# Performance work log

Measured on AMD Instinct MI355X. Metric: run time of the kernel, lower is better.

## Reference

```python
import jax, jax.numpy as jnp
import numpy as np

B, S, D, H = 4, 1024, 1024, 16
HD = D // H


def setup_inputs() -> dict:
    key = jax.random.key(0)
    ks = jax.random.split(key, 8)
    q = jax.random.normal(ks[0], (B, S, D), jnp.float32)
    q_mask = jnp.ones((B, S), dtype=bool)
    kv_mask = jax.random.randint(ks[1], (B, S), 0, 2).astype(bool)
    edge_weights = jax.random.uniform(ks[2], (B, S, S), jnp.float32)
    w_init = 0.02
    wq = jax.random.normal(ks[3], (D, D), jnp.float32) * w_init
    wk = jax.random.normal(ks[4], (D, D), jnp.float32) * w_init
    wv = jax.random.normal(ks[5], (D, D), jnp.float32) * w_init
    wo = jax.random.normal(ks[6], (D, D), jnp.float32) * w_init
    bo = jnp.zeros((D,), jnp.float32)
    return {"q": q, "q_mask": q_mask, "kv_mask": kv_mask,
            "edge_weights": edge_weights, "wq": wq, "wk": wk, "wv": wv,
            "wo": wo, "bo": bo}


def _pass_with_mask(x, w, mask, b=None):
    # Linear applied everywhere, padded rows zeroed (matches pass_with_mask)
    y = x @ w.T
    if b is not None:
        y = y + b
    return jnp.where(mask[..., None], y, 0.0)


def reference(q, q_mask, kv_mask, edge_weights, wq, wk, wv, wo, bo):
    b = q.shape[0]
    # merge_masks: padding mask outer product (recv x send)
    full_mask = (q_mask[:, :, None] & kv_mask[:, None, :])[:, None]  # [b,1,s,s]
    # projections (self attention: k = v = q)
    qh = _pass_with_mask(q, wq, q_mask).reshape(b, S, H, HD).transpose(0, 2, 1, 3)
    kh = _pass_with_mask(q, wk, kv_mask).reshape(b, S, H, HD).transpose(0, 2, 1, 3)
    vh = _pass_with_mask(q, wv, kv_mask).reshape(b, S, H, HD).transpose(0, 2, 1, 3)
    # NOTE: faithful to source, scaled by sqrt(model_dim), not sqrt(head_dim)
    scores = jnp.einsum("bhqd,bhkd->bhqk", qh, kh) / np.sqrt(D).astype(np.float32)
    scores = scores * edge_weights[:, None]          # mul_weights=True
    scores = jnp.where(full_mask, scores, -jnp.inf)
    scores = jax.nn.softmax(scores, axis=-1)
    scores = jnp.where(full_mask, scores, 0.0)       # re-zero masked entries
    out = jnp.einsum("bhqk,bhkd->bhqd", scores, vh)
    out = out.transpose(0, 2, 1, 3).reshape(b, S, D)
    return _pass_with_mask(out, wo, q_mask, bo)
```

## Files before the change

kernel.cpp:

```cpp
#include <hip/hip_runtime.h>

typedef unsigned short u16;
typedef unsigned int u32;
typedef __bf16 b16x8 __attribute__((ext_vector_type(8)));
typedef u16 u16x8 __attribute__((ext_vector_type(8)));
typedef float f32x4 __attribute__((ext_vector_type(4)));
typedef float f32x16 __attribute__((ext_vector_type(16)));
typedef u32 u32x2 __attribute__((ext_vector_type(2)));

#define DEV __device__ __forceinline__
#define INF __builtin_inff()
#define MFMA16(a, b, c) __builtin_amdgcn_mfma_f32_16x16x32_bf16((a), (b), (c), 0, 0, 0)
#define MFMA32(a, b, c) __builtin_amdgcn_mfma_f32_32x32x16_bf16((a), (b), (c), 0, 0, 0)
#define EXP2F(x) __builtin_amdgcn_exp2f(x)

DEV u16 f2b(float f) {
  union { float f; unsigned u; } x; x.f = f;
  unsigned r = x.u + 0x7fffu + ((x.u >> 16) & 1u);
  return (u16)(r >> 16);
}

DEV u32 pk2(float a, float b) {
  __bf16 lo = (__bf16)a, hi = (__bf16)b;
  u16 ul, uh;
  __builtin_memcpy(&ul, &lo, 2);
  __builtin_memcpy(&uh, &hi, 2);
  return (u32)ul | ((u32)uh << 16);
}

DEV float b2f(u16 v) {
  union { u32 u; float f; } x; x.u = (u32)v << 16; return x.f;
}

DEV void gl_lds16(const u16* g, u16* l) {
  __builtin_amdgcn_global_load_lds((const __attribute__((address_space(1))) void*)g,
                                   (__attribute__((address_space(3))) void*)l, 16, 0, 0);
}

__global__ __launch_bounds__(256) void prep_all(const float* __restrict__ q,
                                                const float* __restrict__ wq,
                                                const float* __restrict__ wk,
                                                const float* __restrict__ wv,
                                                const float* __restrict__ wo,
                                                const float* __restrict__ edge,
                                                u16* __restrict__ xb, u16* __restrict__ wqb,
                                                u16* __restrict__ wkb, u16* __restrict__ wvb,
                                                u16* __restrict__ wob, u16* __restrict__ Ef) {
  __shared__ float Ls[32][132];
  const int blk = blockIdx.x;
  const int tid = threadIdx.x;
  if (blk < 8192) {
    const float* src; u16* dst; float scale = 1.f; int base;
    if (blk < 4096)      { src = q;  dst = xb;  base = blk; }
    else if (blk < 5120) { src = wq; dst = wqb; base = blk - 4096; scale = 0.045084441f; }
    else if (blk < 6144) { src = wk; dst = wkb; base = blk - 5120; }
    else if (blk < 7168) { src = wv; dst = wvb; base = blk - 6144; }
    else                 { src = wo; dst = wob; base = blk - 7168; }
    const int i = base * 256 + tid;
    float4 v = reinterpret_cast<const float4*>(src)[i];
    ushort4 o;
    o.x = f2b(v.x * scale);
    o.y = f2b(v.y * scale);
    o.z = f2b(v.z * scale);
    o.w = f2b(v.w * scale);
    reinterpret_cast<ushort4*>(dst)[i] = o;
    return;
  }
  const int rr = blk - 8192;
  const int c = rr & 7, qt = (rr >> 3) & 31, b = rr >> 8;
#pragma unroll
  for (int it = 0; it < 4; ++it) {
    int idx = it * 256 + tid;
    int r = idx >> 5, k4 = idx & 31;
    f32x4 v = *reinterpret_cast<const f32x4*>(
        edge + (size_t)(b * 1024 + qt * 32 + r) * 1024 + c * 128 + k4 * 4);
    *reinterpret_cast<f32x4*>(&Ls[r][k4 * 4]) = v;
  }
  __syncthreads();
#pragma unroll
  for (int it = 0; it < 2; ++it) {
    int slot = it * 256 + tid;
    int kvtl = slot >> 7, i = (slot >> 6) & 1, lane = slot & 63;
    int qv = lane & 31, hi = lane >> 5;
    u16x8 o;
#pragma unroll
    for (int jp = 0; jp < 8; ++jp) {
      int j = i * 8 + jp;
      int kvl = (j & 3) + 8 * (j >> 2) + 4 * hi;
      o[jp] = f2b(Ls[qv][kvtl * 32 + kvl]);
    }
    *reinterpret_cast<u16x8*>(
        Ef + ((size_t)(b * 32 + qt) * 32 + (c * 4 + kvtl)) * 1024 + i * 512 + lane * 8) = o;
  }
}

template <int MODE>
DEV void gemm_body(u16* __restrict__ SA, u16* __restrict__ SB, int m0, int n0,
                   const u16* __restrict__ A, const u16* __restrict__ W,
                   u16* __restrict__ Ybf, float* __restrict__ Yf,
                   const float* __restrict__ bias, const int* __restrict__ qmask) {
  const int t = threadIdx.x;
  const int lane = t & 63, w = t >> 6;
  const int lr = lane & 15, lg = lane >> 4;
  const int wr = w >> 1, wc = w & 1;

  f32x4 acc[4][4] = {};

  const int r0 = t >> 2;
  const int xw = (r0 >> 1) & 3;
  const int c0 = (((t & 3) ^ xw)) * 8;
  const int xa = (lr >> 1) & 3;
  const u16* gA = A + (size_t)(m0 + r0) * 1024 + c0;
  const u16* gB = W + (size_t)(n0 + r0) * 1024 + c0;

  auto stage = [&](int buf, int kt) {
    const int ko = kt * 32;
    u16* lA = SA + buf * 4096 + w * 512;
    u16* lB = SB + buf * 4096 + w * 512;
    gl_lds16(gA + ko, lA);
    gl_lds16(gA + ko + 64 * 1024, lA + 2048);
    gl_lds16(gB + ko, lB);
    gl_lds16(gB + ko + 64 * 1024, lB + 2048);
  };

  stage(0, 0);
  __syncthreads();
  for (int kt = 0; kt < 32; ++kt) {
    const int cur = kt & 1;
    if (kt < 31) stage(cur ^ 1, kt + 1);
    const u16* As = SA + cur * 4096;
    const u16* Bs = SB + cur * 4096;
    b16x8 af[4], bf[4];
#pragma unroll
    for (int m = 0; m < 4; ++m)
      af[m] = *reinterpret_cast<const b16x8*>(As + (wr * 64 + m * 16 + lr) * 32 + ((lg ^ xa) * 8));
#pragma unroll
    for (int n = 0; n < 4; ++n)
      bf[n] = *reinterpret_cast<const b16x8*>(Bs + (wc * 64 + n * 16 + lr) * 32 + ((lg ^ xa) * 8));
#pragma unroll
    for (int m = 0; m < 4; ++m)
#pragma unroll
      for (int n = 0; n < 4; ++n)
        acc[m][n] = MFMA16(af[m], bf[n], acc[m][n]);
    __syncthreads();
  }

#pragma unroll
  for (int m = 0; m < 4; ++m) {
    const int row = m0 + wr * 64 + m * 16 + lg * 4;
#pragma unroll
    for (int n = 0; n < 4; ++n) {
      const int col = n0 + wc * 64 + n * 16 + lr;
#pragma unroll
      for (int r = 0; r < 4; ++r) {
        const int rowg = row + r;
        const float v = acc[m][n][r];
        if (MODE == 3) {
          float y = v + bias[col];
          Yf[(size_t)rowg * 1024 + col] = qmask[rowg] ? y : 0.f;
        } else if (MODE == 1) {
          const int bb = rowg >> 10, rw = rowg & 1023, rt = rw >> 5, rl = rw & 31;
          const int h = col >> 6, dh = col & 63;
          const int s = dh >> 4, hi = (dh >> 3) & 1, j = dh & 7;
          size_t idx = (((size_t)((bb * 16 + h) * 32 + rt) * 4 + s) * 64 + (rl + (hi << 5))) * 8 + j;
          Ybf[idx] = f2b(v);
        } else {
          const int bb = rowg >> 10, kv = rowg & 1023, kvt = kv >> 5, kvl = kv & 31;
          const int s = kvl >> 4, k16 = kvl & 15;
          const int hi = (k16 >> 2) & 1;
          const int j = (k16 & 3) | (((k16 >> 3) & 1) << 2);
          const int h = col >> 6, dh = col & 63, d = dh >> 5;
          size_t idx = ((((size_t)((bb * 16 + h) * 32 + kvt) * 2 + d) * 2 + s) * 64 + ((dh & 31) + (hi << 5))) * 8 + j;
          Ybf[idx] = f2b(v);
        }
      }
    }
  }
}

__global__ __launch_bounds__(256, 4) void gemm_qkv(const u16* __restrict__ X,
                                                   const u16* __restrict__ Wq,
                                                   const u16* __restrict__ Wk,
                                                   const u16* __restrict__ Wv,
                                                   u16* __restrict__ Yq, u16* __restrict__ Yk,
                                                   u16* __restrict__ Yv) {
  __shared__ __attribute__((aligned(16))) u16 SA[2 * 4096];
  __shared__ __attribute__((aligned(16))) u16 SB[2 * 4096];
  const int id = blockIdx.x;
  const int swz = (id & 7) * 96 + (id >> 3);
  const int z = swz >> 8, rem = swz & 255;
  const int by = rem >> 3, bx = rem & 7;
  const int m0 = by * 128, n0 = bx * 128;
  if (z == 0)      gemm_body<1>(SA, SB, m0, n0, X, Wq, Yq, nullptr, nullptr, nullptr);
  else if (z == 1) gemm_body<1>(SA, SB, m0, n0, X, Wk, Yk, nullptr, nullptr, nullptr);
  else             gemm_body<2>(SA, SB, m0, n0, X, Wv, Yv, nullptr, nullptr, nullptr);
}
__global__ __launch_bounds__(256, 4) void gemm_final(const u16* __restrict__ A,
                                                     const u16* __restrict__ Wo,
                                                     float* __restrict__ Out,
                                                     const float* __restrict__ bias,
                                                     const int* __restrict__ qmask) {
  __shared__ __attribute__((aligned(16))) u16 SA[2 * 4096];
  __shared__ __attribute__((aligned(16))) u16 SB[2 * 4096];
  const int id = blockIdx.x;
  const int swz = (id & 7) * 32 + (id >> 3);
  const int by = swz >> 3, bx = swz & 7;
  gemm_body<3>(SA, SB, by * 128, bx * 128, A, Wo, nullptr, Out, bias, qmask);
}

__global__ __launch_bounds__(256, 2) void attn_kernel(
    const u16* __restrict__ Qf, const u16* __restrict__ Kf,
    const u16* __restrict__ Vf, const u16* __restrict__ Ef,
    const int* __restrict__ kvm, u16* __restrict__ out) {
  __shared__ float Osh[3][64][33];
  __shared__ float Lsh[4][32];
  __shared__ __attribute__((aligned(16))) u16 Fsh[1024];

  const int d0 = blockIdx.x;
  const int logical = (d0 & 7) * 256 + (d0 >> 3);
  const int qt = logical & 31, bh = logical >> 5;
  const int b = bh >> 4, h = bh & 15;
  const int tid = threadIdx.x, lane = tid & 63, w = tid >> 6;
  const int ql = lane & 31, hi = lane >> 5;
  const int qrow = qt * 32 + ql;

#pragma unroll
  for (int e = 0; e < 4; ++e) {
    int idx = tid * 4 + e;
    int kt = idx >> 5, h2 = (idx >> 4) & 1, j = idx & 15;
    int kv = kt * 32 + 8 * (j >> 2) + 4 * h2 + (j & 3);
    Fsh[idx] = kvm[b * 1024 + kv] ? (u16)0 : (u16)0xFF80;
  }

  const u16* qp = Qf + (size_t)bh * 65536 + qt * 2048 + lane * 8;
  b16x8 Qr[4];
#pragma unroll
  for (int s = 0; s < 4; ++s) Qr[s] = *reinterpret_cast<const b16x8*>(qp + s * 512);

  const u16* kp = Kf + (size_t)bh * 65536 + lane * 8;
  const u16* vp = Vf + (size_t)bh * 65536 + lane * 8;
  const u16* ep = Ef + (size_t)(b * 32 + qt) * 32768 + lane * 8;

  f32x16 O0 = {}, O1 = {};
  float La[4] = {};

  struct KB { b16x8 K[4]; };
  struct EB { u16x8 E[2]; };
  KB Ka, Kb;
  EB E0, E1, E2, E3;

  auto fK = [&](KB& T, int kvt) {
#pragma unroll
    for (int s = 0; s < 4; ++s)
      T.K[s] = *reinterpret_cast<const b16x8*>(kp + kvt * 2048 + s * 512);
  };
  auto fE = [&](EB& T, int kvt) {
#pragma unroll
    for (int i = 0; i < 2; ++i)
      T.E[i] = *reinterpret_cast<const u16x8*>(ep + kvt * 1024 + i * 512);
  };

  auto compute = [&](const KB& K, const EB& E, int kvt) {
    b16x8 V[4];
#pragma unroll
    for (int ds = 0; ds < 4; ++ds)
      V[ds] = *reinterpret_cast<const b16x8*>(vp + kvt * 2048 + ds * 512);
    u16x8 Fm0 = *reinterpret_cast<const u16x8*>(&Fsh[kvt * 32 + hi * 16]);
    u16x8 Fm1 = *reinterpret_cast<const u16x8*>(&Fsh[kvt * 32 + hi * 16 + 8]);
    f32x16 S = {};
#pragma unroll
    for (int s = 0; s < 4; ++s) S = MFMA32(K.K[s], Qr[s], S);
    float p[16];
#pragma unroll
    for (int j = 0; j < 8; ++j)
      p[j] = EXP2F(fmaf(S[j], b2f(E.E[0][j]), b2f(Fm0[j])));
#pragma unroll
    for (int j = 0; j < 8; ++j)
      p[8 + j] = EXP2F(fmaf(S[8 + j], b2f(E.E[1][j]), b2f(Fm1[j])));
#pragma unroll
    for (int j = 0; j < 16; ++j) La[j & 3] += p[j];
#pragma unroll
    for (int s = 0; s < 2; ++s) {
      union { u32 wd[4]; b16x8 v; } U;
      U.wd[0] = pk2(p[8 * s + 0], p[8 * s + 1]);
      U.wd[1] = pk2(p[8 * s + 2], p[8 * s + 3]);
      U.wd[2] = pk2(p[8 * s + 4], p[8 * s + 5]);
      U.wd[3] = pk2(p[8 * s + 6], p[8 * s + 7]);
      O0 = MFMA32(V[s], U.v, O0);
      O1 = MFMA32(V[2 + s], U.v, O1);
    }
  };

  const int base = w * 8;
  fE(E0, base); fE(E1, base + 1); fE(E2, base + 2);
  fK(Ka, base);
  __syncthreads();

  fE(E3, base + 3); fK(Kb, base + 1); compute(Ka, E0, base + 0);
  fE(E0, base + 4); fK(Ka, base + 2); compute(Kb, E1, base + 1);
  fE(E1, base + 5); fK(Kb, base + 3); compute(Ka, E2, base + 2);
  fE(E2, base + 6); fK(Ka, base + 4); compute(Kb, E3, base + 3);
  fE(E3, base + 7); fK(Kb, base + 5); compute(Ka, E0, base + 4);
                    fK(Ka, base + 6); compute(Kb, E1, base + 5);
                    fK(Kb, base + 7); compute(Ka, E2, base + 6);
                                      compute(Kb, E3, base + 7);

  float Lw = (La[0] + La[1]) + (La[2] + La[3]);
  Lw += __shfl_xor(Lw, 32, 64);

  if (hi == 0) Lsh[w][ql] = Lw;
  if (w > 0) {
#pragma unroll
    for (int r = 0; r < 16; ++r) Osh[w - 1][lane][r] = O0[r];
#pragma unroll
    for (int r = 0; r < 16; ++r) Osh[w - 1][lane][16 + r] = O1[r];
  }
  __syncthreads();
  if (w == 0) {
    float Lg = (Lsh[0][ql] + Lsh[1][ql]) + (Lsh[2][ql] + Lsh[3][ql]);
#pragma unroll
    for (int wv = 0; wv < 3; ++wv) {
#pragma unroll
      for (int r = 0; r < 16; ++r) O0[r] += Osh[wv][lane][r];
#pragma unroll
      for (int r = 0; r < 16; ++r) O1[r] += Osh[wv][lane][16 + r];
    }
    const float inv = (Lg > 0.f) ? 1.f / Lg : 0.f;
    u16* orow = out + (size_t)(b * 1024 + qrow) * 1024 + h * 64 + hi * 4;
#pragma unroll
    for (int H = 0; H < 2; ++H) {
#pragma unroll
      for (int g = 0; g < 4; ++g) {
        float o0 = (H ? O1[4 * g + 0] : O0[4 * g + 0]) * inv;
        float o1 = (H ? O1[4 * g + 1] : O0[4 * g + 1]) * inv;
        float o2 = (H ? O1[4 * g + 2] : O0[4 * g + 2]) * inv;
        float o3 = (H ? O1[4 * g + 3] : O0[4 * g + 3]) * inv;
        u32x2 wv2 = {pk2(o0, o1), pk2(o2, o3)};
        *reinterpret_cast<u32x2*>(orow + H * 32 + g * 8) = wv2;
      }
    }
  }
}

extern "C" void kernel_launch(void* const* d_in, const int* in_sizes, int n_in,
                              void* d_out, int out_size, void* d_ws, size_t ws_size,
                              hipStream_t stream) {
  (void)in_sizes; (void)n_in; (void)out_size; (void)ws_size;
  const float* q    = (const float*)d_in[0];
  const int*   qm   = (const int*)d_in[1];
  const int*   kvm  = (const int*)d_in[2];
  const float* edge = (const float*)d_in[3];
  const float* wq   = (const float*)d_in[4];
  const float* wk   = (const float*)d_in[5];
  const float* wv   = (const float*)d_in[6];
  const float* wo   = (const float*)d_in[7];
  const float* bo   = (const float*)d_in[8];
  float* out = (float*)d_out;

  char* ws = (char*)d_ws;
  u16* xb  = (u16*)(ws);
  u16* wqb = (u16*)(ws + (8ull  << 20));
  u16* wkb = (u16*)(ws + (10ull << 20));
  u16* wvb = (u16*)(ws + (12ull << 20));
  u16* wob = (u16*)(ws + (14ull << 20));
  u16* Qfb = (u16*)(ws + (16ull << 20));
  u16* Kf  = (u16*)(ws + (24ull << 20));
  u16* Vf  = (u16*)(ws + (32ull << 20));
  u16* Ef  = (u16*)(ws + (40ull << 20));
  u16* ab  = xb;

  prep_all<<<9216, 256, 0, stream>>>(q, wq, wk, wv, wo, edge,
                                     xb, wqb, wkb, wvb, wob, Ef);
  gemm_qkv<<<768, 256, 0, stream>>>(xb, wqb, wkb, wvb, Qfb, Kf, Vf);
  attn_kernel<<<2048, 256, 0, stream>>>(Qfb, Kf, Vf, Ef, kvm, ab);
  gemm_final<<<256, 256, 0, stream>>>(ab, wob, out, bo, qm);
}
```

Measured before the change: 112.0 us.

## Move edge-weight repacking into QKV GEMM launch and use 64-row tiles for output GEMM

The edge-weight bf16 repack blocks move out of the conversion kernel and are appended as extra blocks to the QKV GEMM launch, so they run alongside the GEMM tiles instead of serially before them. Shared memory is unified into one buffer so both roles fit. The final output projection becomes a dedicated kernel with 64x128 tiles and 512 blocks instead of 256 blocks of 128x128, giving better CU coverage on a 256-CU part at the cost of reloading each B tile twice as often.

```diff
diff --git a/kernel.cpp b/kernel.cpp
--- a/kernel.cpp
+++ b/kernel.cpp
@@ -37,68 +37,35 @@
                                    (__attribute__((address_space(3))) void*)l, 16, 0, 0);
 }
 
-__global__ __launch_bounds__(256) void prep_all(const float* __restrict__ q,
-                                                const float* __restrict__ wq,
-                                                const float* __restrict__ wk,
-                                                const float* __restrict__ wv,
-                                                const float* __restrict__ wo,
-                                                const float* __restrict__ edge,
-                                                u16* __restrict__ xb, u16* __restrict__ wqb,
-                                                u16* __restrict__ wkb, u16* __restrict__ wvb,
-                                                u16* __restrict__ wob, u16* __restrict__ Ef) {
-  __shared__ float Ls[32][132];
+__global__ __launch_bounds__(256) void cvt_all(const float* __restrict__ q,
+                                               const float* __restrict__ wq,
+                                               const float* __restrict__ wk,
+                                               const float* __restrict__ wv,
+                                               const float* __restrict__ wo,
+                                               u16* __restrict__ xb, u16* __restrict__ wqb,
+                                               u16* __restrict__ wkb, u16* __restrict__ wvb,
+                                               u16* __restrict__ wob) {
   const int blk = blockIdx.x;
-  const int tid = threadIdx.x;
-  if (blk < 8192) {
-    const float* src; u16* dst; float scale = 1.f; int base;
-    if (blk < 4096)      { src = q;  dst = xb;  base = blk; }
-    else if (blk < 5120) { src = wq; dst = wqb; base = blk - 4096; scale = 0.045084441f; }
-    else if (blk < 6144) { src = wk; dst = wkb; base = blk - 5120; }
-    else if (blk < 7168) { src = wv; dst = wvb; base = blk - 6144; }
-    else                 { src = wo; dst = wob; base = blk - 7168; }
-    const int i = base * 256 + tid;
-    float4 v = reinterpret_cast<const float4*>(src)[i];
-    ushort4 o;
-    o.x = f2b(v.x * scale);
-    o.y = f2b(v.y * scale);
-    o.z = f2b(v.z * scale);
-    o.w = f2b(v.w * scale);
-    reinterpret_cast<ushort4*>(dst)[i] = o;
-    return;
-  }
-  const int rr = blk - 8192;
-  const int c = rr & 7, qt = (rr >> 3) & 31, b = rr >> 8;
-#pragma unroll
-  for (int it = 0; it < 4; ++it) {
-    int idx = it * 256 + tid;
-    int r = idx >> 5, k4 = idx & 31;
-    f32x4 v = *reinterpret_cast<const f32x4*>(
-        edge + (size_t)(b * 1024 + qt * 32 + r) * 1024 + c * 128 + k4 * 4);
-    *reinterpret_cast<f32x4*>(&Ls[r][k4 * 4]) = v;
-  }
-  __syncthreads();
-#pragma unroll
-  for (int it = 0; it < 2; ++it) {
-    int slot = it * 256 + tid;
-    int kvtl = slot >> 7, i = (slot >> 6) & 1, lane = slot & 63;
-    int qv = lane & 31, hi = lane >> 5;
-    u16x8 o;
-#pragma unroll
-    for (int jp = 0; jp < 8; ++jp) {
-      int j = i * 8 + jp;
-      int kvl = (j & 3) + 8 * (j >> 2) + 4 * hi;
-      o[jp] = f2b(Ls[qv][kvtl * 32 + kvl]);
-    }
-    *reinterpret_cast<u16x8*>(
-        Ef + ((size_t)(b * 32 + qt) * 32 + (c * 4 + kvtl)) * 1024 + i * 512 + lane * 8) = o;
-  }
+  const float* src; u16* dst; float scale = 1.f; int base;
+  if (blk < 4096)      { src = q;  dst = xb;  base = blk; }
+  else if (blk < 5120) { src = wq; dst = wqb; base = blk - 4096; scale = 0.045084441f; }
+  else if (blk < 6144) { src = wk; dst = wkb; base = blk - 5120; }
+  else if (blk < 7168) { src = wv; dst = wvb; base = blk - 6144; }
+  else                 { src = wo; dst = wob; base = blk - 7168; }
+  const int i = base * 256 + threadIdx.x;
+  float4 v = reinterpret_cast<const float4*>(src)[i];
+  ushort4 o;
+  o.x = f2b(v.x * scale);
+  o.y = f2b(v.y * scale);
+  o.z = f2b(v.z * scale);
+  o.w = f2b(v.w * scale);
+  reinterpret_cast<ushort4*>(dst)[i] = o;
 }
 
 template <int MODE>
 DEV void gemm_body(u16* __restrict__ SA, u16* __restrict__ SB, int m0, int n0,
                    const u16* __restrict__ A, const u16* __restrict__ W,
-                   u16* __restrict__ Ybf, float* __restrict__ Yf,
-                   const float* __restrict__ bias, const int* __restrict__ qmask) {
+                   u16* __restrict__ Ybf) {
   const int t = threadIdx.x;
   const int lane = t & 63, w = t >> 6;
   const int lr = lane & 15, lg = lane >> 4;
@@ -155,10 +122,7 @@
       for (int r = 0; r < 4; ++r) {
         const int rowg = row + r;
         const float v = acc[m][n][r];
-        if (MODE == 3) {
-          float y = v + bias[col];
-          Yf[(size_t)rowg * 1024 + col] = qmask[rowg] ? y : 0.f;
-        } else if (MODE == 1) {
+        if (MODE == 1) {
           const int bb = rowg >> 10, rw = rowg & 1023, rt = rw >> 5, rl = rw & 31;
           const int h = col >> 6, dh = col & 63;
           const int s = dh >> 4, hi = (dh >> 3) & 1, j = dh & 7;
@@ -183,29 +147,122 @@
                                                    const u16* __restrict__ Wk,
                                                    const u16* __restrict__ Wv,
                                                    u16* __restrict__ Yq, u16* __restrict__ Yk,
-                                                   u16* __restrict__ Yv) {
-  __shared__ __attribute__((aligned(16))) u16 SA[2 * 4096];
-  __shared__ __attribute__((aligned(16))) u16 SB[2 * 4096];
+                                                   u16* __restrict__ Yv,
+                                                   const float* __restrict__ edge,
+                                                   u16* __restrict__ Ef) {
+  __shared__ __attribute__((aligned(16))) u16 SU[4 * 4096];
   const int id = blockIdx.x;
+  const int tid = threadIdx.x;
+  if (id >= 768) {
+    float (*Ls)[132] = reinterpret_cast<float(*)[132]>(SU);
+    const int rr = id - 768;
+    const int c = rr & 7, qt = (rr >> 3) & 31, b = rr >> 8;
+#pragma unroll
+    for (int it = 0; it < 4; ++it) {
+      int idx = it * 256 + tid;
+      int r = idx >> 5, k4 = idx & 31;
+      f32x4 v = *reinterpret_cast<const f32x4*>(
+          edge + (size_t)(b * 1024 + qt * 32 + r) * 1024 + c * 128 + k4 * 4);
+      *reinterpret_cast<f32x4*>(&Ls[r][k4 * 4]) = v;
+    }
+    __syncthreads();
+#pragma unroll
+    for (int it = 0; it < 2; ++it) {
+      int slot = it * 256 + tid;
+      int kvtl = slot >> 7, i = (slot >> 6) & 1, lane = slot & 63;
+      int qv = lane & 31, hi = lane >> 5;
+      u16x8 o;
+#pragma unroll
+      for (int jp = 0; jp < 8; ++jp) {
+        int j = i * 8 + jp;
+        int kvl = (j & 3) + 8 * (j >> 2) + 4 * hi;
+        o[jp] = f2b(Ls[qv][kvtl * 32 + kvl]);
+      }
+      *reinterpret_cast<u16x8*>(
+          Ef + ((size_t)(b * 32 + qt) * 32 + (c * 4 + kvtl)) * 1024 + i * 512 + lane * 8) = o;
+    }
+    return;
+  }
+  u16* SA = SU;
+  u16* SB = SU + 2 * 4096;
   const int swz = (id & 7) * 96 + (id >> 3);
   const int z = swz >> 8, rem = swz & 255;
   const int by = rem >> 3, bx = rem & 7;
   const int m0 = by * 128, n0 = bx * 128;
-  if (z == 0)      gemm_body<1>(SA, SB, m0, n0, X, Wq, Yq, nullptr, nullptr, nullptr);
-  else if (z == 1) gemm_body<1>(SA, SB, m0, n0, X, Wk, Yk, nullptr, nullptr, nullptr);
-  else             gemm_body<2>(SA, SB, m0, n0, X, Wv, Yv, nullptr, nullptr, nullptr);
-}
-__global__ __launch_bounds__(256, 4) void gemm_final(const u16* __restrict__ A,
-                                                     const u16* __restrict__ Wo,
-                                                     float* __restrict__ Out,
-                                                     const float* __restrict__ bias,
-                                                     const int* __restrict__ qmask) {
-  __shared__ __attribute__((aligned(16))) u16 SA[2 * 4096];
+  if (z == 0)      gemm_body<1>(SA, SB, m0, n0, X, Wq, Yq);
+  else if (z == 1) gemm_body<1>(SA, SB, m0, n0, X, Wk, Yk);
+  else             gemm_body<2>(SA, SB, m0, n0, X, Wv, Yv);
+}
+
+__global__ __launch_bounds__(256, 4) void gemm_final64(const u16* __restrict__ A,
+                                                       const u16* __restrict__ Wo,
+                                                       float* __restrict__ Out,
+                                                       const float* __restrict__ bias,
+                                                       const int* __restrict__ qmask) {
+  __shared__ __attribute__((aligned(16))) u16 SA[2 * 2048];
   __shared__ __attribute__((aligned(16))) u16 SB[2 * 4096];
   const int id = blockIdx.x;
-  const int swz = (id & 7) * 32 + (id >> 3);
+  const int swz = (id & 7) * 64 + (id >> 3);
   const int by = swz >> 3, bx = swz & 7;
-  gemm_body<3>(SA, SB, by * 128, bx * 128, A, Wo, nullptr, Out, bias, qmask);
+  const int m0 = by * 64, n0 = bx * 128;
+  const int t = threadIdx.x;
+  const int lane = t & 63, w = t >> 6;
+  const int lr = lane & 15, lg = lane >> 4;
+  const int wr = w >> 1, wc = w & 1;
+
+  f32x4 acc[2][4] = {};
+
+  const int r0 = t >> 2;
+  const int xw = (r0 >> 1) & 3;
+  const int c0 = (((t & 3) ^ xw)) * 8;
+  const int xa = (lr >> 1) & 3;
+  const u16* gA = A + (size_t)(m0 + r0) * 1024 + c0;
+  const u16* gB = Wo + (size_t)(n0 + r0) * 1024 + c0;
+
+  auto stage = [&](int buf, int kt) {
+    const int ko = kt * 32;
+    u16* lA = SA + buf * 2048 + w * 512;
+    u16* lB = SB + buf * 4096 + w * 512;
+    gl_lds16(gA + ko, lA);
+    gl_lds16(gB + ko, lB);
+    gl_lds16(gB + ko + 64 * 1024, lB + 2048);
+  };
+
+  stage(0, 0);
+  __syncthreads();
+  for (int kt = 0; kt < 32; ++kt) {
+    const int cur = kt & 1;
+    if (kt < 31) stage(cur ^ 1, kt + 1);
+    const u16* As = SA + cur * 2048;
+    const u16* Bs = SB + cur * 4096;
+    b16x8 af[2], bf[4];
+#pragma unroll
+    for (int m = 0; m < 2; ++m)
+      af[m] = *reinterpret_cast<const b16x8*>(As + (wr * 32 + m * 16 + lr) * 32 + ((lg ^ xa) * 8));
+#pragma unroll
+    for (int n = 0; n < 4; ++n)
+      bf[n] = *reinterpret_cast<const b16x8*>(Bs + (wc * 64 + n * 16 + lr) * 32 + ((lg ^ xa) * 8));
+#pragma unroll
+    for (int m = 0; m < 2; ++m)
+#pragma unroll
+      for (int n = 0; n < 4; ++n)
+        acc[m][n] = MFMA16(af[m], bf[n], acc[m][n]);
+    __syncthreads();
+  }
+
+#pragma unroll
+  for (int m = 0; m < 2; ++m) {
+    const int row = m0 + wr * 32 + m * 16 + lg * 4;
+#pragma unroll
+    for (int n = 0; n < 4; ++n) {
+      const int col = n0 + wc * 64 + n * 16 + lr;
+#pragma unroll
+      for (int r = 0; r < 4; ++r) {
+        float y = acc[m][n][r] + bias[col];
+        Out[(size_t)(row + r) * 1024 + col] = qmask[row + r] ? y : 0.f;
+      }
+    }
+  }
 }
 
 __global__ __launch_bounds__(256, 2) void attn_kernel(
@@ -369,9 +426,8 @@
   u16* Ef  = (u16*)(ws + (40ull << 20));
   u16* ab  = xb;
 
-  prep_all<<<9216, 256, 0, stream>>>(q, wq, wk, wv, wo, edge,
-                                     xb, wqb, wkb, wvb, wob, Ef);
-  gemm_qkv<<<768, 256, 0, stream>>>(xb, wqb, wkb, wvb, Qfb, Kf, Vf);
+  cvt_all<<<8192, 256, 0, stream>>>(q, wq, wk, wv, wo, xb, wqb, wkb, wvb, wob);
+  gemm_qkv<<<1792, 256, 0, stream>>>(xb, wqb, wkb, wvb, Qfb, Kf, Vf, edge, Ef);
   attn_kernel<<<2048, 256, 0, stream>>>(Qfb, Kf, Vf, Ef, kvm, ab);
-  gemm_final<<<256, 256, 0, stream>>>(ab, wob, out, bo, qm);
-}
+  gemm_final64<<<512, 256, 0, stream>>>(ab, wob, out, bo, qm);
+}
```

New measurement: 104.5 us (median of 2 runs). -6.8%, faster.
